# Kernel optimization log

Measured on AMD Instinct MI355X. Metric: run time of the kernel, lower is better.

## Reference

```python
import jax, jax.numpy as jnp
import numpy as np
from jax import lax

K = 3            # kernel_size
STRIDE = 2
PADDING = 1
OUT_PADDING = 1
DILATION = 1


def setup_inputs() -> dict:
    key = jax.random.key(0)
    x = jax.random.normal(key, (16, 64, 64, 64), dtype=jnp.float32)
    return {"x": x}


def _unfold_transpose2d(x):
    """im2col for transpose convolution via one-hot grouped conv-transpose.

    Matches torch.nn.functional.conv_transpose2d(x, W, stride, padding,
    output_padding, dilation, groups=C) with W[c, h*K+w, h, w] = 1 (one-hot),
    followed by reshape to [B, C*K*K, L].
    """
    B, C, H, W = x.shape
    KK = K * K
    # One-hot kernel: [KK, 1, K, K], tiled per input channel -> [C*KK, 1, K, K]
    eye = jnp.eye(KK, dtype=x.dtype).reshape(KK, 1, K, K)
    weight = jnp.tile(eye, (C, 1, 1, 1))
    # conv_transpose == conv with lhs dilation and spatially flipped kernel
    w_flip = weight[:, :, ::-1, ::-1]
    pad_lo = DILATION * (K - 1) - PADDING
    pad_hi = pad_lo + OUT_PADDING
    out = lax.conv_general_dilated(
        x,
        w_flip,
        window_strides=(1, 1),
        padding=[(pad_lo, pad_hi), (pad_lo, pad_hi)],
        lhs_dilation=(STRIDE, STRIDE),
        rhs_dilation=(DILATION, DILATION),
        dimension_numbers=("NCHW", "OIHW", "NCHW"),
        feature_group_count=C,
    )  # [B, C*KK, H_out, W_out]
    return out.reshape(B, C * KK, -1)


def reference(x):
    return _unfold_transpose2d(x)
```

## Files before the change

kernel.cpp:

```cpp
#include <hip/hip_runtime.h>


#define C_ 64
#define HW_ 64
#define OW_ 128
#define OH_ 128
#define KK_ 9

__global__ __launch_bounds__(256) void unfold_t2d_kernel(
    const float* __restrict__ x, float* __restrict__ out, int n4) {
    int i4 = blockIdx.x * 256 + threadIdx.x;
    if (i4 >= n4) return;

    int ow0 = (i4 & 31) << 2;
    int row = i4 >> 5;
    int oh  = row & 127;
    int t   = row >> 7;
    int j   = t % 9;
    int cc  = t / 9;
    int jh  = j / 3;
    int jw  = j - jh * 3;

    int rh = oh + 1 - jh;
    int ih = rh >> 1;
    bool vh = (rh >= 0) & ((rh & 1) == 0) & (ih < HW_);

    float4 o = make_float4(0.f, 0.f, 0.f, 0.f);
    if (vh) {
        const float* xrow = x + (cc * HW_ + ih) * HW_;
        float* po = &o.x;
#pragma unroll
        for (int q = 0; q < 4; ++q) {
            int rw = ow0 + q + 1 - jw;
            int iw = rw >> 1;
            if (rw >= 0 && (rw & 1) == 0 && iw < HW_) {
                po[q] = xrow[iw];
            }
        }
    }
    reinterpret_cast<float4*>(out)[i4] = o;
}

extern "C" void kernel_launch(void* const* d_in, const int* in_sizes, int n_in,
                              void* d_out, int out_size, void* d_ws, size_t ws_size,
                              hipStream_t stream) {
    const float* x = (const float*)d_in[0];
    float* out = (float*)d_out;
    int n4 = out_size >> 2;
    int blocks = (n4 + 255) / 256;
    unfold_t2d_kernel<<<blocks, 256, 0, stream>>>(x, out, n4);
}
```

Measured before the change: 618.6 us.

## Assign one wavefront per channel-tap plane and loop over output rows

Restructures the unfold kernel so each wavefront owns a full (batch-channel, tap) output plane and iterates over 128 output rows, each lane writing a float2 covering two output columns. Column parity and source offsets are computed once per wave instead of per element, cutting index math and redundant per-thread decoding. The cost is narrower float2 stores instead of float4 and serialized row stores per wave, which may reduce achieved write bandwidth for this store-bound kernel.

```diff
diff --git a/kernel.cpp b/kernel.cpp
--- a/kernel.cpp
+++ b/kernel.cpp
@@ -1,44 +1,34 @@
 #include <hip/hip_runtime.h>
 
 
-#define C_ 64
-#define HW_ 64
-#define OW_ 128
-#define OH_ 128
-#define KK_ 9
+__global__ __launch_bounds__(256) void unfold_t2d_kernel(
+    const float* __restrict__ x, float* __restrict__ out) {
+    int lane = threadIdx.x & 63;
+    int wid  = blockIdx.x * 4 + (threadIdx.x >> 6);
+    int cc   = wid / 9;
+    int j    = wid - cc * 9;
+    int jh   = j / 3;
+    int jw   = j - jh * 3;
+    int p    = (1 - jw) & 1;
+    int dlt  = (jw == 0) ? 1 : 0;
+    int iwl  = lane + dlt;
+    bool wv  = iwl < 64;
 
-__global__ __launch_bounds__(256) void unfold_t2d_kernel(
-    const float* __restrict__ x, float* __restrict__ out, int n4) {
-    int i4 = blockIdx.x * 256 + threadIdx.x;
-    if (i4 >= n4) return;
+    const float* xc = x + cc * 4096;
+    float2* ob = reinterpret_cast<float2*>(out + ((size_t)wid << 14)) + lane;
 
-    int ow0 = (i4 & 31) << 2;
-    int row = i4 >> 5;
-    int oh  = row & 127;
-    int t   = row >> 7;
-    int j   = t % 9;
-    int cc  = t / 9;
-    int jh  = j / 3;
-    int jw  = j - jh * 3;
-
-    int rh = oh + 1 - jh;
-    int ih = rh >> 1;
-    bool vh = (rh >= 0) & ((rh & 1) == 0) & (ih < HW_);
-
-    float4 o = make_float4(0.f, 0.f, 0.f, 0.f);
-    if (vh) {
-        const float* xrow = x + (cc * HW_ + ih) * HW_;
-        float* po = &o.x;
-#pragma unroll
-        for (int q = 0; q < 4; ++q) {
-            int rw = ow0 + q + 1 - jw;
-            int iw = rw >> 1;
-            if (rw >= 0 && (rw & 1) == 0 && iw < HW_) {
-                po[q] = xrow[iw];
-            }
-        }
+#pragma unroll 4
+    for (int oh = 0; oh < 128; ++oh) {
+        int rh = oh + 1 - jh;
+        int ih = rh >> 1;
+        bool hv = (rh >= 0) & ((rh & 1) == 0) & (ih < 64);
+        float v = 0.f;
+        if (hv & wv) v = xc[ih * 64 + iwl];
+        float2 o;
+        o.x = (p == 0) ? v : 0.f;
+        o.y = (p == 1) ? v : 0.f;
+        ob[(size_t)oh * 64] = o;
     }
-    reinterpret_cast<float4*>(out)[i4] = o;
 }
 
 extern "C" void kernel_launch(void* const* d_in, const int* in_sizes, int n_in,
@@ -46,7 +36,5 @@
                               hipStream_t stream) {
     const float* x = (const float*)d_in[0];
     float* out = (float*)d_out;
-    int n4 = out_size >> 2;
-    int blocks = (n4 + 255) / 256;
-    unfold_t2d_kernel<<<blocks, 256, 0, stream>>>(x, out, n4);
+    unfold_t2d_kernel<<<2304, 256, 0, stream>>>(x, out);
 }
```

Measured after the change: 662.4 us. 7.1% more time.
